# Performance work log

Hardware: AMD Instinct MI355X
Metric: run time of the kernel (lower is better)

## Reference

```python
import jax, jax.numpy as jnp
import numpy as np

B, C, H, W = 32, 256, 32, 32

def conv1x1(x, w, b):
    # x: [b,c,h,w], w: [out,in], b: [out]  (1x1 conv == per-pixel linear)
    return jnp.einsum('bchw,oc->bohw', x, w) + b[None, :, None, None]

def setup_inputs() -> dict:
    key = jax.random.key(0)
    ks = jax.random.split(key, 16)
    scale = 1.0 / np.sqrt(C)
    def wgt(k):
        return jax.random.normal(k, (C, C), dtype=jnp.float32) * scale
    def bia(k):
        return jax.random.normal(k, (C,), dtype=jnp.float32) * 0.01
    return {
        'x1': jax.random.normal(ks[0], (B, C, H, W), dtype=jnp.float32),
        'x2': jax.random.normal(ks[1], (B, C, H, W), dtype=jnp.float32),
        'wq1': wgt(ks[2]), 'bq1': bia(ks[3]),
        'wk': wgt(ks[4]), 'bk': bia(ks[5]),
        'wv': wgt(ks[6]), 'bv': bia(ks[7]),
        'wq2': wgt(ks[8]), 'bq2': bia(ks[9]),
        'wps': wgt(ks[10]), 'bps': bia(ks[11]),
        'wpc': wgt(ks[12]), 'bpc': bia(ks[13]),
    }

def reference(x1, x2, wq1, bq1, wk, bk, wv, bv, wq2, bq2, wps, bps, wpc, bpc):
    b, c, h, w = x1.shape
    hw = h * w
    inv_sqrt_c = c ** (-0.5)

    def tokens(t):  # [b,c,h,w] -> [b,hw,c]  (matches permute(0,2,3,1).view)
        return jnp.transpose(t, (0, 2, 3, 1)).reshape(b, hw, c)

    q1 = tokens(conv1x1(x1, wq1, bq1))
    k = tokens(conv1x1(x1, wk, bk))
    v = tokens(conv1x1(x1, wv, bv))  # [b,hw,c]

    # self-attention scores: [b, q_tokens, k_tokens]
    w1 = jnp.einsum('bqc,bkc->bqk', q1, k) * inv_sqrt_c
    a1 = jax.nn.softmax(w1, axis=-1)
    h1 = jnp.einsum('bqk,bkc->bqc', a1, v)  # [b,hw,c]
    h1 = jnp.transpose(h1, (0, 2, 1)).reshape(b, c, h, w)
    h1 = conv1x1(h1, wps, bps)

    # cross-attention: q from x2, shared k/v from x1, scores added
    q2 = tokens(conv1x1(x2, wq2, bq2))
    w2 = jnp.einsum('bqc,bkc->bqk', q2, k) * inv_sqrt_c
    a12 = jax.nn.softmax(w1 + w2, axis=-1)
    h12 = jnp.einsum('bqk,bkc->bqc', a12, v)
    h12 = jnp.transpose(h12, (0, 2, 1)).reshape(b, c, h, w)
    h12 = conv1x1(h12, wpc, bpc)

    return (x1 + h1, x1 + h12)
```

## Files before the change

### kernel.cpp

```cpp
#include <hip/hip_runtime.h>
#include <math.h>

#define Bn 32
#define Cn 256
#define Pn 1024
#define Tn (Bn * Pn * Cn)

typedef __bf16 bf16x8 __attribute__((ext_vector_type(8)));
typedef float  f32x4  __attribute__((ext_vector_type(4)));
typedef unsigned short u16;
typedef u16 u16x8 __attribute__((ext_vector_type(8)));

#define XT1o ((size_t)0)
#define XT2o ((size_t)1 * Tn)
#define Q1o  ((size_t)2 * Tn)
#define Ko   ((size_t)3 * Tn)
#define VTo  ((size_t)4 * Tn)
#define Q2o  ((size_t)5 * Tn)
#define H1o  ((size_t)6 * Tn)
#define H12o ((size_t)7 * Tn)
#define WBo  ((size_t)8 * Tn)

__device__ __forceinline__ u16 f2b(float f) {
    union { float f; unsigned u; } c; c.f = f;
    return (u16)((c.u + 0x7FFFu + ((c.u >> 16) & 1u)) >> 16);
}

__global__ __launch_bounds__(256) void cvt_kernel(
    const float* __restrict__ x1, const float* __restrict__ x2,
    const float* __restrict__ wq1, const float* __restrict__ wk,
    const float* __restrict__ wv,  const float* __restrict__ wq2,
    const float* __restrict__ wps, const float* __restrict__ wpc,
    u16* __restrict__ ws16)
{
    const int z = blockIdx.z;
    const int tid = threadIdx.x;
    if (z >= 64) {
        const int widx = z - 64;
        const float* w = widx == 0 ? wq1 : widx == 1 ? wk : widx == 2 ? wv
                       : widx == 3 ? wq2 : widx == 4 ? wps : wpc;
        const int linear = blockIdx.x + 16 * blockIdx.y;
        const int e = linear * 1024 + tid * 4;
        float4 v = *(const float4*)&w[e];
        ushort4 o = make_ushort4(f2b(v.x), f2b(v.y), f2b(v.z), f2b(v.w));
        *(ushort4*)&ws16[WBo + (size_t)widx * 65536 + e] = o;
        return;
    }
    const int which = z >> 5, b = z & 31;
    const float* x = which ? x2 : x1;
    u16* xt = ws16 + (which ? XT2o : XT1o);
    const int p0 = blockIdx.x * 64, c0 = blockIdx.y * 64;
    __shared__ __align__(16) u16 T[64][80];
    #pragma unroll
    for (int i = 0; i < 4; i++) {
        int e = tid + i * 256;
        int c = e >> 4, p4 = e & 15;
        float4 v = *(const float4*)&x[((size_t)(b * Cn + c0 + c)) * Pn + p0 + p4 * 4];
        T[p4 * 4 + 0][c] = f2b(v.x);
        T[p4 * 4 + 1][c] = f2b(v.y);
        T[p4 * 4 + 2][c] = f2b(v.z);
        T[p4 * 4 + 3][c] = f2b(v.w);
    }
    __syncthreads();
    #pragma unroll
    for (int i = 0; i < 2; i++) {
        int e = tid + i * 256;
        int p = e >> 3, c8 = e & 7;
        u16x8 vv = *(const u16x8*)&T[p][c8 * 8];
        *(u16x8*)&xt[((size_t)(b * Pn + p0 + p)) * Cn + c0 + c8 * 8] = vv;
    }
}

__device__ __forceinline__ void gemm_core(
    const u16* __restrict__ Ab, const u16* __restrict__ Bb,
    u16* __restrict__ As, u16* __restrict__ Bs, f32x4 acc[16], int tid)
{
    const int wv = tid >> 6, lane = tid & 63;
    const int ln = lane & 15, quad = lane >> 4;
    const int wr = wv >> 1, wc = wv & 1;
    const int srow = tid >> 3, sch = tid & 7;
    const int pos = sch ^ (srow & 7);

    u16x8 apre[4], bpre[4];
    #pragma unroll
    for (int i = 0; i < 4; i++) {
        int r = srow + 32 * i;
        apre[i] = *(const u16x8*)&Ab[(size_t)r * 256 + sch * 8];
        bpre[i] = *(const u16x8*)&Bb[(size_t)r * 256 + sch * 8];
    }

    for (int k0 = 0; k0 < 256; k0 += 64) {
        __syncthreads();
        #pragma unroll
        for (int i = 0; i < 4; i++) {
            int r = srow + 32 * i;
            *(u16x8*)&As[r * 64 + pos * 8] = apre[i];
            *(u16x8*)&Bs[r * 64 + pos * 8] = bpre[i];
        }
        __syncthreads();
        if (k0 < 192) {
            #pragma unroll
            for (int i = 0; i < 4; i++) {
                int r = srow + 32 * i;
                apre[i] = *(const u16x8*)&Ab[(size_t)r * 256 + (k0 + 64) + sch * 8];
                bpre[i] = *(const u16x8*)&Bb[(size_t)r * 256 + (k0 + 64) + sch * 8];
            }
        }
        bf16x8 af[4][2], bf[4][2];
        #pragma unroll
        for (int i = 0; i < 4; i++) {
            int row = wr * 64 + i * 16 + ln;
            #pragma unroll
            for (int kc = 0; kc < 2; kc++) {
                int p = (kc * 4 + quad) ^ (row & 7);
                af[i][kc] = *(const bf16x8*)&As[row * 64 + p * 8];
            }
        }
        #pragma unroll
        for (int j = 0; j < 4; j++) {
            int row = wc * 64 + j * 16 + ln;
            #pragma unroll
            for (int kc = 0; kc < 2; kc++) {
                int p = (kc * 4 + quad) ^ (row & 7);
                bf[j][kc] = *(const bf16x8*)&Bs[row * 64 + p * 8];
            }
        }
        #pragma unroll
        for (int kc = 0; kc < 2; kc++)
            #pragma unroll
            for (int i = 0; i < 4; i++)
                #pragma unroll
                for (int j = 0; j < 4; j++)
                    acc[i * 4 + j] = __builtin_amdgcn_mfma_f32_16x16x32_bf16(
                        af[i][kc], bf[j][kc], acc[i * 4 + j], 0, 0, 0);
    }
}

__global__ __launch_bounds__(256) void proj_kernel(
    u16* __restrict__ ws16,
    const float* __restrict__ bq1, const float* __restrict__ bk,
    const float* __restrict__ bq2, const float* __restrict__ bv)
{
    __shared__ __align__(16) u16 As[128 * 64];
    __shared__ __align__(16) u16 Bs[128 * 64];
    const int tid = threadIdx.x;
    const int mat = blockIdx.y;
    const int wv = tid >> 6, lane = tid & 63;
    const int ln = lane & 15, quad = lane >> 4;
    const int wr = wv >> 1, wc = wv & 1;

    f32x4 acc[16];
    #pragma unroll
    for (int t = 0; t < 16; t++) acc[t] = (f32x4){0.f, 0.f, 0.f, 0.f};

    if (mat < 3) {
        const int m_tile = blockIdx.x >> 1, n_tile = blockIdx.x & 1;
        const size_t xtoff = (mat == 2) ? XT2o : XT1o;
        const int widx = (mat == 0) ? 0 : (mat == 1) ? 1 : 3;
        const float* bias = (mat == 0) ? bq1 : (mat == 1) ? bk : bq2;
        const float scale = (mat == 1) ? 1.0f : 0.0625f;
        u16* out = ws16 + ((mat == 0) ? Q1o : (mat == 1) ? Ko : Q2o);

        const u16* Ab = ws16 + xtoff + (size_t)m_tile * 128 * 256;
        const u16* Bb = ws16 + WBo + (size_t)widx * 65536 + (size_t)n_tile * 128 * 256;
        gemm_core(Ab, Bb, As, Bs, acc, tid);

        const int m0 = m_tile * 128;
        #pragma unroll
        for (int j = 0; j < 4; j++) {
            const int ncol = n_tile * 128 + wc * 64 + j * 16 + ln;
            const float bj = bias[ncol];
            #pragma unroll
            for (int i = 0; i < 4; i++) {
                const int mr = m0 + wr * 64 + i * 16 + quad * 4;
                #pragma unroll
                for (int r = 0; r < 4; r++)
                    out[(size_t)(mr + r) * 256 + ncol] =
                        f2b((acc[i * 4 + j][r] + bj) * scale);
            }
        }
    } else {
        const int b = blockIdx.x >> 4;
        const int o_tile = (blockIdx.x >> 3) & 1;
        const int p_tile = blockIdx.x & 7;
        const u16* Ab = ws16 + WBo + (size_t)2 * 65536 + (size_t)o_tile * 128 * 256;
        const u16* Bb = ws16 + XT1o + ((size_t)b * Pn + p_tile * 128) * 256;
        gemm_core(Ab, Bb, As, Bs, acc, tid);

        u16* vt = ws16 + VTo + (size_t)b * Cn * Pn;
        #pragma unroll
        for (int i = 0; i < 4; i++) {
            #pragma unroll
            for (int r = 0; r < 4; r++) {
                const int orow = o_tile * 128 + wr * 64 + i * 16 + quad * 4 + r;
                const float bo = bv[orow];
                #pragma unroll
                for (int j = 0; j < 4; j++) {
                    const int pcol = p_tile * 128 + wc * 64 + j * 16 + ln;
                    vt[(size_t)orow * Pn + pcol] = f2b(acc[i * 4 + j][r] + bo);
                }
            }
        }
    }
}

__global__ __launch_bounds__(256, 2) void attn_kernel(u16* __restrict__ ws16)
{
    const u16* Q1 = ws16 + Q1o;
    const u16* Kg = ws16 + Ko;
    const u16* Vt = ws16 + VTo;
    const u16* Q2 = ws16 + Q2o;

    __shared__ __align__(16) u16 Klds[32 * 256];
    __shared__ __align__(16) u16 Vtlds[256 * 32];
    __shared__ __align__(16) u16 Plds[4 * 2 * 16 * 40];

    const int b    = blockIdx.y;
    const int q0   = blockIdx.x * 64;
    const int tid  = threadIdx.x;
    const int wid  = tid >> 6;
    const int lane = tid & 63;
    const int ln   = lane & 15;
    const int quad = lane >> 4;
    u16* Pw = Plds + wid * (2 * 16 * 40);

    const size_t qrow = (size_t)(b * Pn + q0 + wid * 16 + ln) * Cn;
    bf16x8 qa1[8], qa2[8];
    #pragma unroll
    for (int ch = 0; ch < 8; ch++) {
        qa1[ch] = *(const bf16x8*)&Q1[qrow + ch * 32 + quad * 8];
        qa2[ch] = *(const bf16x8*)&Q2[qrow + ch * 32 + quad * 8];
    }

    f32x4 acc1[16], acc12[16];
    #pragma unroll
    for (int t = 0; t < 16; t++) {
        acc1[t] = (f32x4){0.f, 0.f, 0.f, 0.f};
        acc12[t] = (f32x4){0.f, 0.f, 0.f, 0.f};
    }
    float lp1[4] = {}, lp12[4] = {};

    const int tokK = tid >> 3, giK = tid & 7;
    const int cbV = tid >> 2, gvV = tid & 3;
    u16x8 kpre[4], vpre[4];

    {
        const size_t growK = (size_t)(b * Pn + 0 + tokK) * Cn;
        #pragma unroll
        for (int i = 0; i < 4; i++)
            kpre[i] = *(const u16x8*)&Kg[growK + (size_t)(8 * i + (giK ^ (tokK & 7))) * 8];
        #pragma unroll
        for (int i = 0; i < 4; i++) {
            int cl = cbV + 64 * i;
            vpre[i] = *(const u16x8*)&Vt[((size_t)(b * Cn + cl)) * Pn + 0 + gvV * 8];
        }
    }

    for (int kt = 0; kt < 32; kt++) {
        __syncthreads();

        #pragma unroll
        for (int i = 0; i < 4; i++)
            *(u16x8*)&Klds[tokK * 256 + (8 * i + giK) * 8] = kpre[i];
        #pragma unroll
        for (int i = 0; i < 4; i++) {
            int cl = cbV + 64 * i;
            int gp = gvV ^ (cl & 3);
            *(u16x8*)&Vtlds[cl * 32 + gp * 8] = vpre[i];
        }
        __syncthreads();

        if (kt < 31) {
            const int k0n = (kt + 1) * 32;
            const size_t growK = (size_t)(b * Pn + k0n + tokK) * Cn;
            #pragma unroll
            for (int i = 0; i < 4; i++)
                kpre[i] = *(const u16x8*)&Kg[growK + (size_t)(8 * i + (giK ^ (tokK & 7))) * 8];
            #pragma unroll
            for (int i = 0; i < 4; i++) {
                int cl = cbV + 64 * i;
                vpre[i] = *(const u16x8*)&Vt[((size_t)(b * Cn + cl)) * Pn + k0n + gvV * 8];
            }
        }

        float s1v[2][4], s2v[2][4];
        #pragma unroll
        for (int st = 0; st < 2; st++) {
            f32x4 s1 = (f32x4){0.f, 0.f, 0.f, 0.f};
            f32x4 s2 = (f32x4){0.f, 0.f, 0.f, 0.f};
            #pragma unroll
            for (int ch = 0; ch < 8; ch++) {
                bf16x8 kb = *(const bf16x8*)
                    &Klds[(st * 16 + ln) * 256 + (((ch * 4 + quad) ^ (ln & 7))) * 8];
                s1 = __builtin_amdgcn_mfma_f32_16x16x32_bf16(qa1[ch], kb, s1, 0, 0, 0);
                s2 = __builtin_amdgcn_mfma_f32_16x16x32_bf16(qa2[ch], kb, s2, 0, 0, 0);
            }
            #pragma unroll
            for (int r = 0; r < 4; r++) { s1v[st][r] = s1[r]; s2v[st][r] = s2[r]; }
        }

        #pragma unroll
        for (int st = 0; st < 2; st++)
            #pragma unroll
            for (int r = 0; r < 4; r++) {
                float p1 = __expf(s1v[st][r]);
                float p12 = p1 * __expf(s2v[st][r]);
                lp1[r] += p1;
                lp12[r] += p12;
                int row = quad * 4 + r, col = st * 16 + ln;
                Pw[row * 40 + col]            = f2b(p1);
                Pw[16 * 40 + row * 40 + col]  = f2b(p12);
            }

        bf16x8 pa1 = *(const bf16x8*)&Pw[ln * 40 + quad * 8];
        bf16x8 pa2 = *(const bf16x8*)&Pw[16 * 40 + ln * 40 + quad * 8];
        #pragma unroll
        for (int t = 0; t < 16; t++) {
            bf16x8 vb = *(const bf16x8*)
                &Vtlds[(t * 16 + ln) * 32 + (quad ^ (ln & 3)) * 8];
            acc1[t]  = __builtin_amdgcn_mfma_f32_16x16x32_bf16(pa1, vb, acc1[t], 0, 0, 0);
            acc12[t] = __builtin_amdgcn_mfma_f32_16x16x32_bf16(pa2, vb, acc12[t], 0, 0, 0);
        }
    }

    u16* H1 = ws16 + H1o;
    u16* H12 = ws16 + H12o;
    #pragma unroll
    for (int r = 0; r < 4; r++) {
        float l1 = lp1[r], l2 = lp12[r];
        l1 += __shfl_xor(l1, 1); l2 += __shfl_xor(l2, 1);
        l1 += __shfl_xor(l1, 2); l2 += __shfl_xor(l2, 2);
        l1 += __shfl_xor(l1, 4); l2 += __shfl_xor(l2, 4);
        l1 += __shfl_xor(l1, 8); l2 += __shfl_xor(l2, 8);
        float i1 = 1.f / l1, i2 = 1.f / l2;
        size_t rowb = (size_t)(b * Pn + q0 + wid * 16 + quad * 4 + r) * Cn;
        #pragma unroll
        for (int t = 0; t < 16; t++) {
            H1[rowb + t * 16 + ln]  = f2b(acc1[t][r] * i1);
            H12[rowb + t * 16 + ln] = f2b(acc12[t][r] * i2);
        }
    }
}

__global__ __launch_bounds__(256) void outproj_kernel(
    const float* __restrict__ x1,
    const float* __restrict__ bps, const float* __restrict__ bpc,
    const u16* __restrict__ ws16, float* __restrict__ outp)
{
    __shared__ __align__(16) u16 As[128 * 64];
    __shared__ __align__(16) u16 Bs[128 * 64];
    const int tid = threadIdx.x;
    const int o_tile = blockIdx.x >> 3, p_tile = blockIdx.x & 7;
    const int mat = blockIdx.y >> 5, b = blockIdx.y & 31;
    const int wv = tid >> 6, lane = tid & 63;
    const int ln = lane & 15, quad = lane >> 4;
    const int wr = wv >> 1, wc = wv & 1;

    f32x4 acc[16];
    #pragma unroll
    for (int t = 0; t < 16; t++) acc[t] = (f32x4){0.f, 0.f, 0.f, 0.f};

    const u16* Ab = ws16 + WBo + (size_t)(4 + mat) * 65536 + (size_t)o_tile * 128 * 256;
    const u16* Bb = ws16 + (mat ? H12o : H1o) + ((size_t)b * Pn + p_tile * 128) * 256;
    gemm_core(Ab, Bb, As, Bs, acc, tid);

    const float* bias = mat ? bpc : bps;
    float* out = outp + (size_t)mat * Tn;
    #pragma unroll
    for (int i = 0; i < 4; i++) {
        #pragma unroll
        for (int r = 0; r < 4; r++) {
            const int orow = o_tile * 128 + wr * 64 + i * 16 + quad * 4 + r;
            const float bo = bias[orow];
            #pragma unroll
            for (int j = 0; j < 4; j++) {
                const int pcol = p_tile * 128 + wc * 64 + j * 16 + ln;
                const size_t idx = ((size_t)b * Cn + orow) * Pn + pcol;
                out[idx] = x1[idx] + bo + acc[i * 4 + j][r];
            }
        }
    }
}

extern "C" void kernel_launch(void* const* d_in, const int* in_sizes, int n_in,
                              void* d_out, int out_size, void* d_ws, size_t ws_size,
                              hipStream_t stream)
{
    const float* x1  = (const float*)d_in[0];
    const float* x2  = (const float*)d_in[1];
    const float* wq1 = (const float*)d_in[2];
    const float* bq1 = (const float*)d_in[3];
    const float* wk  = (const float*)d_in[4];
    const float* bk  = (const float*)d_in[5];
    const float* wv  = (const float*)d_in[6];
    const float* bv  = (const float*)d_in[7];
    const float* wq2 = (const float*)d_in[8];
    const float* bq2 = (const float*)d_in[9];
    const float* wps = (const float*)d_in[10];
    const float* bps = (const float*)d_in[11];
    const float* wpc = (const float*)d_in[12];
    const float* bpc = (const float*)d_in[13];
    float* out = (float*)d_out;
    u16* ws16 = (u16*)d_ws;

    cvt_kernel<<<dim3(16, 4, 70), 256, 0, stream>>>(
        x1, x2, wq1, wk, wv, wq2, wps, wpc, ws16);
    proj_kernel<<<dim3(512, 4), 256, 0, stream>>>(ws16, bq1, bk, bq2, bv);
    attn_kernel<<<dim3(Pn / 64, Bn), 256, 0, stream>>>(ws16);
    outproj_kernel<<<dim3(16, 64), 256, 0, stream>>>(x1, bps, bpc, ws16, out);
}
```

Measured before the change: 300.4 us.

## Fuse output projection and residual add into attention kernel epilogue

The attention kernel now stages its normalized H1/H12 tiles in a swizzled shared-memory buffer and runs the 256x256 output projection GEMM in-block, adding bias and the x1 residual before writing the final outputs. The separate outproj kernel and the bf16 H1/H12 round-trip through global memory are removed. In exchange, each attention block reads the full projection weights from global/L2 without LDS staging, uses an extra 32KB of LDS that may reduce occupancy, and holds a second set of accumulators, which adds register pressure.

```diff
diff --git a/kernel.cpp b/kernel.cpp
--- a/kernel.cpp
+++ b/kernel.cpp
@@ -204,7 +204,10 @@
     }
 }
 
-__global__ __launch_bounds__(256, 2) void attn_kernel(u16* __restrict__ ws16)
+__global__ __launch_bounds__(256, 2) void attn_kernel(
+    u16* __restrict__ ws16, const float* __restrict__ x1,
+    const float* __restrict__ bps, const float* __restrict__ bpc,
+    float* __restrict__ outp)
 {
     const u16* Q1 = ws16 + Q1o;
     const u16* Kg = ws16 + Ko;
@@ -214,6 +217,7 @@
     __shared__ __align__(16) u16 Klds[32 * 256];
     __shared__ __align__(16) u16 Vtlds[256 * 32];
     __shared__ __align__(16) u16 Plds[4 * 2 * 16 * 40];
+    __shared__ __align__(16) u16 Hlds[64 * 256];
 
     const int b    = blockIdx.y;
     const int q0   = blockIdx.x * 64;
@@ -323,8 +327,7 @@
         }
     }
 
-    u16* H1 = ws16 + H1o;
-    u16* H12 = ws16 + H12o;
+    float inv1[4], inv2[4];
     #pragma unroll
     for (int r = 0; r < 4; r++) {
         float l1 = lp1[r], l2 = lp12[r];
@@ -332,53 +335,67 @@
         l1 += __shfl_xor(l1, 2); l2 += __shfl_xor(l2, 2);
         l1 += __shfl_xor(l1, 4); l2 += __shfl_xor(l2, 4);
         l1 += __shfl_xor(l1, 8); l2 += __shfl_xor(l2, 8);
-        float i1 = 1.f / l1, i2 = 1.f / l2;
-        size_t rowb = (size_t)(b * Pn + q0 + wid * 16 + quad * 4 + r) * Cn;
-        #pragma unroll
-        for (int t = 0; t < 16; t++) {
-            H1[rowb + t * 16 + ln]  = f2b(acc1[t][r] * i1);
-            H12[rowb + t * 16 + ln] = f2b(acc12[t][r] * i2);
-        }
-    }
-}
-
-__global__ __launch_bounds__(256) void outproj_kernel(
-    const float* __restrict__ x1,
-    const float* __restrict__ bps, const float* __restrict__ bpc,
-    const u16* __restrict__ ws16, float* __restrict__ outp)
-{
-    __shared__ __align__(16) u16 As[128 * 64];
-    __shared__ __align__(16) u16 Bs[128 * 64];
-    const int tid = threadIdx.x;
-    const int o_tile = blockIdx.x >> 3, p_tile = blockIdx.x & 7;
-    const int mat = blockIdx.y >> 5, b = blockIdx.y & 31;
-    const int wv = tid >> 6, lane = tid & 63;
-    const int ln = lane & 15, quad = lane >> 4;
-    const int wr = wv >> 1, wc = wv & 1;
-
-    f32x4 acc[16];
-    #pragma unroll
-    for (int t = 0; t < 16; t++) acc[t] = (f32x4){0.f, 0.f, 0.f, 0.f};
-
-    const u16* Ab = ws16 + WBo + (size_t)(4 + mat) * 65536 + (size_t)o_tile * 128 * 256;
-    const u16* Bb = ws16 + (mat ? H12o : H1o) + ((size_t)b * Pn + p_tile * 128) * 256;
-    gemm_core(Ab, Bb, As, Bs, acc, tid);
-
-    const float* bias = mat ? bpc : bps;
-    float* out = outp + (size_t)mat * Tn;
-    #pragma unroll
-    for (int i = 0; i < 4; i++) {
-        #pragma unroll
-        for (int r = 0; r < 4; r++) {
-            const int orow = o_tile * 128 + wr * 64 + i * 16 + quad * 4 + r;
-            const float bo = bias[orow];
-            #pragma unroll
-            for (int j = 0; j < 4; j++) {
-                const int pcol = p_tile * 128 + wc * 64 + j * 16 + ln;
-                const size_t idx = ((size_t)b * Cn + orow) * Pn + pcol;
-                out[idx] = x1[idx] + bo + acc[i * 4 + j][r];
-            }
-        }
+        inv1[r] = 1.f / l1;
+        inv2[r] = 1.f / l2;
+    }
+
+    const u16* Wps = ws16 + WBo + (size_t)4 * 65536;
+    const u16* Wpc = ws16 + WBo + (size_t)5 * 65536;
+
+    for (int path = 0; path < 2; path++) {
+        __syncthreads();
+        #pragma unroll
+        for (int t = 0; t < 16; t++)
+            #pragma unroll
+            for (int r = 0; r < 4; r++) {
+                const int q = wid * 16 + quad * 4 + r;
+                const int lc = t * 2 + (ln >> 3);
+                const float v = path ? acc12[t][r] * inv2[r]
+                                     : acc1[t][r] * inv1[r];
+                Hlds[q * 256 + ((lc ^ (q & 7)) * 8) + (ln & 7)] = f2b(v);
+            }
+        __syncthreads();
+
+        const u16* W = path ? Wpc : Wps;
+        const float* bias = path ? bpc : bps;
+        f32x4 acc2[16];
+        #pragma unroll
+        for (int t = 0; t < 16; t++) acc2[t] = (f32x4){0.f, 0.f, 0.f, 0.f};
+
+        #pragma unroll
+        for (int kb = 0; kb < 8; kb++) {
+            bf16x8 aw[4], bh[4];
+            #pragma unroll
+            for (int o4 = 0; o4 < 4; o4++)
+                aw[o4] = *(const bf16x8*)
+                    &W[(size_t)(wid * 64 + o4 * 16 + ln) * 256 + kb * 32 + quad * 8];
+            #pragma unroll
+            for (int p4 = 0; p4 < 4; p4++) {
+                const int prow = p4 * 16 + ln;
+                bh[p4] = *(const bf16x8*)
+                    &Hlds[prow * 256 + (((kb * 4 + quad) ^ (prow & 7)) * 8)];
+            }
+            #pragma unroll
+            for (int o4 = 0; o4 < 4; o4++)
+                #pragma unroll
+                for (int p4 = 0; p4 < 4; p4++)
+                    acc2[o4 * 4 + p4] = __builtin_amdgcn_mfma_f32_16x16x32_bf16(
+                        aw[o4], bh[p4], acc2[o4 * 4 + p4], 0, 0, 0);
+        }
+
+        float* outm = outp + (size_t)path * Tn;
+        #pragma unroll
+        for (int o4 = 0; o4 < 4; o4++)
+            #pragma unroll
+            for (int r = 0; r < 4; r++) {
+                const int o = wid * 64 + o4 * 16 + quad * 4 + r;
+                const float bo = bias[o];
+                #pragma unroll
+                for (int p4 = 0; p4 < 4; p4++) {
+                    const size_t idx = ((size_t)b * Cn + o) * Pn + q0 + p4 * 16 + ln;
+                    outm[idx] = x1[idx] + bo + acc2[o4 * 4 + p4][r];
+                }
+            }
     }
 }
 
@@ -406,6 +423,5 @@
     cvt_kernel<<<dim3(16, 4, 70), 256, 0, stream>>>(
         x1, x2, wq1, wk, wv, wq2, wps, wpc, ws16);
     proj_kernel<<<dim3(512, 4), 256, 0, stream>>>(ws16, bq1, bk, bq2, bv);
-    attn_kernel<<<dim3(Pn / 64, Bn), 256, 0, stream>>>(ws16);
-    outproj_kernel<<<dim3(16, 64), 256, 0, stream>>>(x1, bps, bpc, ws16, out);
-}
+    attn_kernel<<<dim3(Pn / 64, Bn), 256, 0, stream>>>(ws16, x1, bps, bpc, out);
+}
```

New measurement: 384.9 us. +28.1%, slower.
